# Kernel optimization log

Hardware: AMD Instinct MI355X
Metric: run time of the kernel (lower is better)

Reference implementation:

```python
import jax, jax.numpy as jnp
import numpy as np

S = 7          # grid cells per side (CFG['CELL_NUMS'])
L_COORD = 5.0  # CFG['L_COORD']
L_NOOBJ = 0.5  # CFG['L_NOOBJ']
N_BATCH = 16384


def setup_inputs() -> dict:
    key = jax.random.key(0)
    k1, k2, k3 = jax.random.split(key, 3)
    pred = jax.random.uniform(k1, (N_BATCH, S, S, 30), dtype=jnp.float32)
    target = jax.random.uniform(k2, (N_BATCH, S, S, 30), dtype=jnp.float32)
    obj = jax.random.uniform(k3, (N_BATCH, S, S)) < 0.3
    target = target.at[..., 4].set(jnp.where(obj, target[..., 4], 0.0))
    target = target.at[..., 9].set(jnp.where(obj, target[..., 9], 0.0))
    return {"pred_tensor": pred, "target_tensor": target}


def _yolo_v1_loss(pred, target):
    # pred/target: [N, S, S, 30] = [2 boxes x (x,y,w,h,c), 20 class probs]
    N = pred.shape[0]
    coo_f = (target[..., 4] > 0).astype(pred.dtype)   # [N,S,S] object cells
    noo_f = 1.0 - coo_f                                # no-object cells

    # no-object loss: confidence channels 4 and 9 on noo cells (sum-MSE)
    nooobj_loss = jnp.sum(
        noo_f * ((pred[..., 4] - target[..., 4]) ** 2
                 + (pred[..., 9] - target[..., 9]) ** 2))

    # class loss over object cells (sum-MSE over 20 classes)
    class_loss = jnp.sum(coo_f[..., None] * (pred[..., 10:] - target[..., 10:]) ** 2)

    # boxes: [N,S,S,2,5]
    pb = pred[..., :10].reshape(N, S, S, 2, 5)
    tb = target[..., :10].reshape(N, S, S, 2, 5)

    # xywh -> xyxy for the 2 predicted boxes and the first target box per cell
    p_lt = pb[..., :2] - 0.5 * pb[..., 2:4]
    p_rb = pb[..., :2] + 0.5 * pb[..., 2:4]
    t0 = tb[..., 0, :]                                 # target box used for IOU
    t_lt = t0[..., :2] - 0.5 * t0[..., 2:4]
    t_rb = t0[..., :2] + 0.5 * t0[..., 2:4]

    # NOTE: faithful reproduction of the source's compute_iou, including its
    # bug: wh = (rb - lt < 0).float(), so 'inter' is an indicator product.
    lt = jnp.maximum(p_lt, t_lt[..., None, :])         # [N,S,S,2,2]
    rb = jnp.minimum(p_rb, t_rb[..., None, :])
    wh_ind = (rb - lt < 0).astype(pred.dtype)
    inter = wh_ind[..., 0] * wh_ind[..., 1]            # [N,S,S,2]
    area1 = (p_rb[..., 0] - p_lt[..., 0]) * (p_rb[..., 1] - p_lt[..., 1])
    area2 = ((t_rb[..., 0] - t_lt[..., 0]) * (t_rb[..., 1] - t_lt[..., 1]))[..., None]
    iou = inter / (area1 + area2 - inter)              # [N,S,S,2]

    # responsible box = argmax IOU over the 2 predicted boxes per cell
    idx = jnp.argmax(iou, axis=-1)                     # [N,S,S]
    gather = idx[..., None, None]                      # [N,S,S,1,1]
    resp_p = jnp.take_along_axis(pb, gather, axis=3)[..., 0, :]  # [N,S,S,5]
    resp_t = jnp.take_along_axis(tb, gather, axis=3)[..., 0, :]

    contain_loss = jnp.sum(coo_f * (resp_p[..., 4] - resp_t[..., 4]) ** 2)

    # guard sqrt at masked-out cells so 0*d(sqrt(0)) does not produce NaN grads
    safe = coo_f[..., None] > 0
    sqrt_wp = jnp.sqrt(jnp.where(safe, resp_p[..., 2:4], 1.0))
    sqrt_wt = jnp.sqrt(jnp.where(safe, resp_t[..., 2:4], 1.0))
    loc_loss = (jnp.sum(coo_f[..., None] * (resp_p[..., :2] - resp_t[..., :2]) ** 2)
                + jnp.sum(coo_f[..., None] * (sqrt_wp - sqrt_wt) ** 2))

    return (L_COORD * loc_loss + contain_loss + L_NOOBJ * nooobj_loss + class_loss) / N


def reference(pred_tensor, target_tensor):
    return _yolo_v1_loss(pred_tensor, target_tensor)
```

## Files before the change

### kernel.cpp

```cpp
#include <hip/hip_runtime.h>


#define CH 30
#define CELLS_PER_BLOCK 256
#define BLOCK_THREADS 256
#define FLOATS_PER_BLOCK (CELLS_PER_BLOCK * CH)
#define VEC4_PER_BLOCK (FLOATS_PER_BLOCK / 4)
#define N_BATCH_F 16384.0f

__global__ __launch_bounds__(BLOCK_THREADS)
void yolo_partial(const float* __restrict__ pred,
                  const float* __restrict__ targ,
                  float* __restrict__ partial,
                  int n_cells) {
    __shared__ float sp[FLOATS_PER_BLOCK];
    __shared__ float st[FLOATS_PER_BLOCK];
    __shared__ float wave_sums[BLOCK_THREADS / 64];

    const int tid = threadIdx.x;
    const int cell0 = blockIdx.x * CELLS_PER_BLOCK;
    const int ncell_here = min(CELLS_PER_BLOCK, n_cells - cell0);
    const long long fbase = (long long)cell0 * CH;

    if (ncell_here == CELLS_PER_BLOCK) {
        const float4* gp = (const float4*)(pred + fbase);
        const float4* gt = (const float4*)(targ + fbase);
        float4* lp = (float4*)sp;
        float4* lt4 = (float4*)st;
        for (int v = tid; v < VEC4_PER_BLOCK; v += BLOCK_THREADS) {
            lp[v] = gp[v];
            lt4[v] = gt[v];
        }
    } else {
        const int nflt = ncell_here * CH;
        for (int v = tid; v < nflt; v += BLOCK_THREADS) {
            sp[v] = pred[fbase + v];
            st[v] = targ[fbase + v];
        }
    }
    __syncthreads();

    float sum = 0.0f;
    if (tid < ncell_here) {
        const float* p = &sp[tid * CH];
        const float* t = &st[tid * CH];

        const float t4 = t[4];
        const float t9 = t[9];
        const float coo = (t4 > 0.0f) ? 1.0f : 0.0f;
        const float noo = 1.0f - coo;

        {
            const float d4 = p[4] - t4;
            const float d9 = p[9] - t9;
            sum += 0.5f * noo * (d4 * d4 + d9 * d9);
        }

        if (coo > 0.0f) {
            float cl = 0.0f;
#pragma unroll
            for (int c = 10; c < 30; ++c) {
                const float d = p[c] - t[c];
                cl += d * d;
            }
            sum += cl;

            const float t0x = t[0], t0y = t[1], t0w = t[2], t0h = t[3];
            const float tltx = t0x - 0.5f * t0w;
            const float tlty = t0y - 0.5f * t0h;
            const float trbx = t0x + 0.5f * t0w;
            const float trby = t0y + 0.5f * t0h;
            const float area2 = (trbx - tltx) * (trby - tlty);

            float iou0, iou1;
#pragma unroll
            for (int b = 0; b < 2; ++b) {
                const float* pb = p + b * 5;
                const float pltx = pb[0] - 0.5f * pb[2];
                const float plty = pb[1] - 0.5f * pb[3];
                const float prbx = pb[0] + 0.5f * pb[2];
                const float prby = pb[1] + 0.5f * pb[3];
                const float ltx = fmaxf(pltx, tltx);
                const float lty = fmaxf(plty, tlty);
                const float rbx = fminf(prbx, trbx);
                const float rby = fminf(prby, trby);
                const float wind = (rbx - ltx < 0.0f) ? 1.0f : 0.0f;
                const float hind = (rby - lty < 0.0f) ? 1.0f : 0.0f;
                const float inter = wind * hind;
                const float area1 = (prbx - pltx) * (prby - plty);
                const float iou = inter / (area1 + area2 - inter);
                if (b == 0) iou0 = iou; else iou1 = iou;
            }
            const int idx = (iou1 > iou0) ? 1 : 0;
            const float* rp = p + idx * 5;
            const float* rt = t + idx * 5;

            const float dc = rp[4] - rt[4];
            sum += dc * dc;

            const float dx = rp[0] - rt[0];
            const float dy = rp[1] - rt[1];
            const float dw = sqrtf(rp[2]) - sqrtf(rt[2]);
            const float dh = sqrtf(rp[3]) - sqrtf(rt[3]);
            sum += 5.0f * (dx * dx + dy * dy + dw * dw + dh * dh);
        }
    }

#pragma unroll
    for (int off = 32; off > 0; off >>= 1)
        sum += __shfl_down(sum, off, 64);
    const int wave = tid >> 6;
    const int lane = tid & 63;
    if (lane == 0) wave_sums[wave] = sum;
    __syncthreads();
    if (tid == 0) {
        float tot = 0.0f;
#pragma unroll
        for (int w = 0; w < BLOCK_THREADS / 64; ++w) tot += wave_sums[w];
        partial[blockIdx.x] = tot;
    }
}

__global__ __launch_bounds__(256)
void yolo_reduce(const float* __restrict__ partial, int n, float* __restrict__ out) {
    __shared__ float wave_sums[4];
    float s = 0.0f;
    for (int i = threadIdx.x; i < n; i += 256)
        s += partial[i];
#pragma unroll
    for (int off = 32; off > 0; off >>= 1)
        s += __shfl_down(s, off, 64);
    const int wave = threadIdx.x >> 6;
    const int lane = threadIdx.x & 63;
    if (lane == 0) wave_sums[wave] = s;
    __syncthreads();
    if (threadIdx.x == 0) {
        float tot = wave_sums[0] + wave_sums[1] + wave_sums[2] + wave_sums[3];
        out[0] = tot * (1.0f / N_BATCH_F);
    }
}

extern "C" void kernel_launch(void* const* d_in, const int* in_sizes, int n_in,
                              void* d_out, int out_size, void* d_ws, size_t ws_size,
                              hipStream_t stream) {
    const float* pred = (const float*)d_in[0];
    const float* targ = (const float*)d_in[1];
    float* out = (float*)d_out;
    float* partial = (float*)d_ws;

    const int n_cells = in_sizes[0] / CH;
    const int blocks = (n_cells + CELLS_PER_BLOCK - 1) / CELLS_PER_BLOCK;

    yolo_partial<<<blocks, BLOCK_THREADS, 0, stream>>>(pred, targ, partial, n_cells);
    yolo_reduce<<<1, 256, 0, stream>>>(partial, blocks, out);
}
```

Measured before the change: 209.6 us.

## Use direct global-to-LDS loads with a single reused tile and register-held targets

Result: faster. 204.2 us (-2.6%).

```diff
diff --git a/kernel.cpp b/kernel.cpp
--- a/kernel.cpp
+++ b/kernel.cpp
@@ -2,106 +2,130 @@
 
 
 #define CH 30
-#define CELLS_PER_BLOCK 256
-#define BLOCK_THREADS 256
-#define FLOATS_PER_BLOCK (CELLS_PER_BLOCK * CH)
-#define VEC4_PER_BLOCK (FLOATS_PER_BLOCK / 4)
-#define N_BATCH_F 16384.0f
+#define CPB 256
+#define T 256
+#define TILE_F (CPB * CH)
+#define TILE_V4 (TILE_F / 4)
 
-__global__ __launch_bounds__(BLOCK_THREADS)
+typedef __attribute__((address_space(3))) void* lds_vp;
+typedef const __attribute__((address_space(1))) void* gvp;
+
+__global__ __launch_bounds__(T, 4)
 void yolo_partial(const float* __restrict__ pred,
                   const float* __restrict__ targ,
-                  float* __restrict__ partial,
-                  int n_cells) {
-    __shared__ float sp[FLOATS_PER_BLOCK];
-    __shared__ float st[FLOATS_PER_BLOCK];
-    __shared__ float wave_sums[BLOCK_THREADS / 64];
+                  float* __restrict__ partial) {
+    __shared__ float tile[TILE_F];
+    __shared__ float wave_sums[T / 64];
 
     const int tid = threadIdx.x;
-    const int cell0 = blockIdx.x * CELLS_PER_BLOCK;
-    const int ncell_here = min(CELLS_PER_BLOCK, n_cells - cell0);
-    const long long fbase = (long long)cell0 * CH;
+    const long long fbase = (long long)blockIdx.x * TILE_F;
 
-    if (ncell_here == CELLS_PER_BLOCK) {
+    {
+        const float4* gt = (const float4*)(targ + fbase);
+#pragma unroll
+        for (int k = 0; k < 8; ++k) {
+            const int v = tid + k * T;
+            if (v < TILE_V4)
+                __builtin_amdgcn_global_load_lds((gvp)(gt + v), (lds_vp)(tile + v * 4),
+                                                 16, 0, 0);
+        }
+    }
+    __syncthreads();
+
+    float2 t01, t23, t45, t67, t89, tc[10];
+    {
+        const float2* t2 = (const float2*)(tile + tid * CH);
+        t01 = t2[0]; t23 = t2[1]; t45 = t2[2]; t67 = t2[3]; t89 = t2[4];
+#pragma unroll
+        for (int k = 0; k < 10; ++k) tc[k] = t2[5 + k];
+    }
+    __syncthreads();
+
+    {
         const float4* gp = (const float4*)(pred + fbase);
-        const float4* gt = (const float4*)(targ + fbase);
-        float4* lp = (float4*)sp;
-        float4* lt4 = (float4*)st;
-        for (int v = tid; v < VEC4_PER_BLOCK; v += BLOCK_THREADS) {
-            lp[v] = gp[v];
-            lt4[v] = gt[v];
-        }
-    } else {
-        const int nflt = ncell_here * CH;
-        for (int v = tid; v < nflt; v += BLOCK_THREADS) {
-            sp[v] = pred[fbase + v];
-            st[v] = targ[fbase + v];
+#pragma unroll
+        for (int k = 0; k < 8; ++k) {
+            const int v = tid + k * T;
+            if (v < TILE_V4)
+                __builtin_amdgcn_global_load_lds((gvp)(gp + v), (lds_vp)(tile + v * 4),
+                                                 16, 0, 0);
         }
     }
     __syncthreads();
 
     float sum = 0.0f;
-    if (tid < ncell_here) {
-        const float* p = &sp[tid * CH];
-        const float* t = &st[tid * CH];
+    {
+        const float2* p2 = (const float2*)(tile + tid * CH);
+        const float2 p01 = p2[0], p23 = p2[1], p45 = p2[2], p67 = p2[3], p89 = p2[4];
 
-        const float t4 = t[4];
-        const float t9 = t[9];
-        const float coo = (t4 > 0.0f) ? 1.0f : 0.0f;
-        const float noo = 1.0f - coo;
+        const float t4 = t45.x, t9 = t89.y;
+        const bool coo = t4 > 0.0f;
 
-        {
-            const float d4 = p[4] - t4;
-            const float d9 = p[9] - t9;
-            sum += 0.5f * noo * (d4 * d4 + d9 * d9);
-        }
+        const float d4 = p45.x - t4;
+        const float d9 = p89.y - t9;
+        sum = coo ? 0.0f : 0.5f * (d4 * d4 + d9 * d9);
 
-        if (coo > 0.0f) {
+        if (coo) {
             float cl = 0.0f;
 #pragma unroll
-            for (int c = 10; c < 30; ++c) {
-                const float d = p[c] - t[c];
-                cl += d * d;
+            for (int k = 0; k < 10; ++k) {
+                const float2 pc = p2[5 + k];
+                const float dx = pc.x - tc[k].x;
+                const float dy = pc.y - tc[k].y;
+                cl += dx * dx + dy * dy;
             }
             sum += cl;
 
-            const float t0x = t[0], t0y = t[1], t0w = t[2], t0h = t[3];
-            const float tltx = t0x - 0.5f * t0w;
-            const float tlty = t0y - 0.5f * t0h;
-            const float trbx = t0x + 0.5f * t0w;
-            const float trby = t0y + 0.5f * t0h;
+            const float tltx = t01.x - 0.5f * t23.x;
+            const float tlty = t01.y - 0.5f * t23.y;
+            const float trbx = t01.x + 0.5f * t23.x;
+            const float trby = t01.y + 0.5f * t23.y;
             const float area2 = (trbx - tltx) * (trby - tlty);
 
+            const float b0x = p01.x, b0y = p01.y, b0w = p23.x, b0h = p23.y;
+            const float b1x = p45.y, b1y = p67.x, b1w = p67.y, b1h = p89.x;
+
             float iou0, iou1;
-#pragma unroll
-            for (int b = 0; b < 2; ++b) {
-                const float* pb = p + b * 5;
-                const float pltx = pb[0] - 0.5f * pb[2];
-                const float plty = pb[1] - 0.5f * pb[3];
-                const float prbx = pb[0] + 0.5f * pb[2];
-                const float prby = pb[1] + 0.5f * pb[3];
-                const float ltx = fmaxf(pltx, tltx);
-                const float lty = fmaxf(plty, tlty);
-                const float rbx = fminf(prbx, trbx);
-                const float rby = fminf(prby, trby);
-                const float wind = (rbx - ltx < 0.0f) ? 1.0f : 0.0f;
-                const float hind = (rby - lty < 0.0f) ? 1.0f : 0.0f;
-                const float inter = wind * hind;
+            {
+                const float pltx = b0x - 0.5f * b0w, plty = b0y - 0.5f * b0h;
+                const float prbx = b0x + 0.5f * b0w, prby = b0y + 0.5f * b0h;
+                const float ltx = fmaxf(pltx, tltx), lty = fmaxf(plty, tlty);
+                const float rbx = fminf(prbx, trbx), rby = fminf(prby, trby);
+                const float inter = ((rbx - ltx < 0.0f) ? 1.0f : 0.0f) *
+                                    ((rby - lty < 0.0f) ? 1.0f : 0.0f);
                 const float area1 = (prbx - pltx) * (prby - plty);
-                const float iou = inter / (area1 + area2 - inter);
-                if (b == 0) iou0 = iou; else iou1 = iou;
+                iou0 = inter / (area1 + area2 - inter);
             }
-            const int idx = (iou1 > iou0) ? 1 : 0;
-            const float* rp = p + idx * 5;
-            const float* rt = t + idx * 5;
+            {
+                const float pltx = b1x - 0.5f * b1w, plty = b1y - 0.5f * b1h;
+                const float prbx = b1x + 0.5f * b1w, prby = b1y + 0.5f * b1h;
+                const float ltx = fmaxf(pltx, tltx), lty = fmaxf(plty, tlty);
+                const float rbx = fminf(prbx, trbx), rby = fminf(prby, trby);
+                const float inter = ((rbx - ltx < 0.0f) ? 1.0f : 0.0f) *
+                                    ((rby - lty < 0.0f) ? 1.0f : 0.0f);
+                const float area1 = (prbx - pltx) * (prby - plty);
+                iou1 = inter / (area1 + area2 - inter);
+            }
+            const bool idx1 = iou1 > iou0;
 
-            const float dc = rp[4] - rt[4];
+            const float rpx = idx1 ? b1x : b0x;
+            const float rpy = idx1 ? b1y : b0y;
+            const float rpw = idx1 ? b1w : b0w;
+            const float rph = idx1 ? b1h : b0h;
+            const float rpc = idx1 ? p89.y : p45.x;
+            const float rtx = idx1 ? t45.y : t01.x;
+            const float rty = idx1 ? t67.x : t01.y;
+            const float rtw = idx1 ? t67.y : t23.x;
+            const float rth = idx1 ? t89.x : t23.y;
+            const float rtc = idx1 ? t89.y : t45.x;
+
+            const float dc = rpc - rtc;
             sum += dc * dc;
 
-            const float dx = rp[0] - rt[0];
-            const float dy = rp[1] - rt[1];
-            const float dw = sqrtf(rp[2]) - sqrtf(rt[2]);
-            const float dh = sqrtf(rp[3]) - sqrtf(rt[3]);
+            const float dx = rpx - rtx;
+            const float dy = rpy - rty;
+            const float dw = sqrtf(rpw) - sqrtf(rtw);
+            const float dh = sqrtf(rph) - sqrtf(rth);
             sum += 5.0f * (dx * dx + dy * dy + dw * dw + dh * dh);
         }
     }
@@ -116,7 +140,7 @@
     if (tid == 0) {
         float tot = 0.0f;
 #pragma unroll
-        for (int w = 0; w < BLOCK_THREADS / 64; ++w) tot += wave_sums[w];
+        for (int w = 0; w < T / 64; ++w) tot += wave_sums[w];
         partial[blockIdx.x] = tot;
     }
 }
@@ -125,8 +149,14 @@
 void yolo_reduce(const float* __restrict__ partial, int n, float* __restrict__ out) {
     __shared__ float wave_sums[4];
     float s = 0.0f;
-    for (int i = threadIdx.x; i < n; i += 256)
-        s += partial[i];
+    const int n4 = n >> 2;
+    const float4* p4 = (const float4*)partial;
+    for (int v = threadIdx.x; v < n4; v += 256) {
+        const float4 x = p4[v];
+        s += (x.x + x.y) + (x.z + x.w);
+    }
+    for (int v = (n4 << 2) + threadIdx.x; v < n; v += 256)
+        s += partial[v];
 #pragma unroll
     for (int off = 32; off > 0; off >>= 1)
         s += __shfl_down(s, off, 64);
@@ -135,8 +165,8 @@
     if (lane == 0) wave_sums[wave] = s;
     __syncthreads();
     if (threadIdx.x == 0) {
-        float tot = wave_sums[0] + wave_sums[1] + wave_sums[2] + wave_sums[3];
-        out[0] = tot * (1.0f / N_BATCH_F);
+        const float tot = wave_sums[0] + wave_sums[1] + wave_sums[2] + wave_sums[3];
+        out[0] = tot * (1.0f / 16384.0f);
     }
 }
 
@@ -149,8 +179,8 @@
     float* partial = (float*)d_ws;
 
     const int n_cells = in_sizes[0] / CH;
-    const int blocks = (n_cells + CELLS_PER_BLOCK - 1) / CELLS_PER_BLOCK;
+    const int blocks = n_cells / CPB;
 
-    yolo_partial<<<blocks, BLOCK_THREADS, 0, stream>>>(pred, targ, partial, n_cells);
+    yolo_partial<<<blocks, T, 0, stream>>>(pred, targ, partial);
     yolo_reduce<<<1, 256, 0, stream>>>(partial, blocks, out);
 }
```

## Load cell pairs directly into registers via float4, drop shared-memory staging

Applied to the files above, without the earlier changes.

New measurement: 263.2 us. 1.26x slower.

```diff
diff --git a/kernel.cpp b/kernel.cpp
--- a/kernel.cpp
+++ b/kernel.cpp
@@ -2,109 +2,87 @@
 
 
 #define CH 30
-#define CELLS_PER_BLOCK 256
-#define BLOCK_THREADS 256
-#define FLOATS_PER_BLOCK (CELLS_PER_BLOCK * CH)
-#define VEC4_PER_BLOCK (FLOATS_PER_BLOCK / 4)
-#define N_BATCH_F 16384.0f
 
-__global__ __launch_bounds__(BLOCK_THREADS)
+__device__ __forceinline__ float cell_loss(const float* __restrict__ t,
+                                           const float* __restrict__ p) {
+    const float t4 = t[4];
+    const bool coo = t4 > 0.0f;
+
+    const float d4 = p[4] - t4;
+    const float d9 = p[9] - t[9];
+    float sum = coo ? 0.0f : 0.5f * (d4 * d4 + d9 * d9);
+
+    if (coo) {
+        float cl = 0.0f;
+#pragma unroll
+        for (int c = 10; c < 30; ++c) {
+            const float d = p[c] - t[c];
+            cl += d * d;
+        }
+        sum += cl;
+
+        const float tltx = t[0] - 0.5f * t[2];
+        const float tlty = t[1] - 0.5f * t[3];
+        const float trbx = t[0] + 0.5f * t[2];
+        const float trby = t[1] + 0.5f * t[3];
+        const float area2 = (trbx - tltx) * (trby - tlty);
+
+        float iou0, iou1;
+#pragma unroll
+        for (int b = 0; b < 2; ++b) {
+            const float bx = p[b * 5 + 0], by = p[b * 5 + 1];
+            const float bw = p[b * 5 + 2], bh = p[b * 5 + 3];
+            const float pltx = bx - 0.5f * bw, plty = by - 0.5f * bh;
+            const float prbx = bx + 0.5f * bw, prby = by + 0.5f * bh;
+            const float ltx = fmaxf(pltx, tltx), lty = fmaxf(plty, tlty);
+            const float rbx = fminf(prbx, trbx), rby = fminf(prby, trby);
+            const float inter = ((rbx - ltx < 0.0f) ? 1.0f : 0.0f) *
+                                ((rby - lty < 0.0f) ? 1.0f : 0.0f);
+            const float area1 = (prbx - pltx) * (prby - plty);
+            const float iou = inter / (area1 + area2 - inter);
+            if (b == 0) iou0 = iou; else iou1 = iou;
+        }
+        const int o = (iou1 > iou0) ? 5 : 0;
+
+        const float dc = p[o + 4] - t[o + 4];
+        sum += dc * dc;
+
+        const float dx = p[o + 0] - t[o + 0];
+        const float dy = p[o + 1] - t[o + 1];
+        const float dw = sqrtf(p[o + 2]) - sqrtf(t[o + 2]);
+        const float dh = sqrtf(p[o + 3]) - sqrtf(t[o + 3]);
+        sum += 5.0f * (dx * dx + dy * dy + dw * dw + dh * dh);
+    }
+    return sum;
+}
+
+__global__ __launch_bounds__(256, 3)
 void yolo_partial(const float* __restrict__ pred,
                   const float* __restrict__ targ,
-                  float* __restrict__ partial,
-                  int n_cells) {
-    __shared__ float sp[FLOATS_PER_BLOCK];
-    __shared__ float st[FLOATS_PER_BLOCK];
-    __shared__ float wave_sums[BLOCK_THREADS / 64];
+                  float* __restrict__ partial) {
+    __shared__ float wave_sums[4];
 
     const int tid = threadIdx.x;
-    const int cell0 = blockIdx.x * CELLS_PER_BLOCK;
-    const int ncell_here = min(CELLS_PER_BLOCK, n_cells - cell0);
-    const long long fbase = (long long)cell0 * CH;
+    const long long pair = (long long)blockIdx.x * 256 + tid;
 
-    if (ncell_here == CELLS_PER_BLOCK) {
-        const float4* gp = (const float4*)(pred + fbase);
-        const float4* gt = (const float4*)(targ + fbase);
-        float4* lp = (float4*)sp;
-        float4* lt4 = (float4*)st;
-        for (int v = tid; v < VEC4_PER_BLOCK; v += BLOCK_THREADS) {
-            lp[v] = gp[v];
-            lt4[v] = gt[v];
-        }
-    } else {
-        const int nflt = ncell_here * CH;
-        for (int v = tid; v < nflt; v += BLOCK_THREADS) {
-            sp[v] = pred[fbase + v];
-            st[v] = targ[fbase + v];
-        }
+    const float4* t4 = (const float4*)targ + pair * 15;
+    const float4* p4 = (const float4*)pred + pair * 15;
+
+    float tv[60], pv[60];
+#pragma unroll
+    for (int i = 0; i < 15; ++i) {
+        const float4 v = t4[i];
+        tv[4 * i + 0] = v.x; tv[4 * i + 1] = v.y;
+        tv[4 * i + 2] = v.z; tv[4 * i + 3] = v.w;
     }
-    __syncthreads();
+#pragma unroll
+    for (int i = 0; i < 15; ++i) {
+        const float4 v = p4[i];
+        pv[4 * i + 0] = v.x; pv[4 * i + 1] = v.y;
+        pv[4 * i + 2] = v.z; pv[4 * i + 3] = v.w;
+    }
 
-    float sum = 0.0f;
-    if (tid < ncell_here) {
-        const float* p = &sp[tid * CH];
-        const float* t = &st[tid * CH];
-
-        const float t4 = t[4];
-        const float t9 = t[9];
-        const float coo = (t4 > 0.0f) ? 1.0f : 0.0f;
-        const float noo = 1.0f - coo;
-
-        {
-            const float d4 = p[4] - t4;
-            const float d9 = p[9] - t9;
-            sum += 0.5f * noo * (d4 * d4 + d9 * d9);
-        }
-
-        if (coo > 0.0f) {
-            float cl = 0.0f;
-#pragma unroll
-            for (int c = 10; c < 30; ++c) {
-                const float d = p[c] - t[c];
-                cl += d * d;
-            }
-            sum += cl;
-
-            const float t0x = t[0], t0y = t[1], t0w = t[2], t0h = t[3];
-            const float tltx = t0x - 0.5f * t0w;
-            const float tlty = t0y - 0.5f * t0h;
-            const float trbx = t0x + 0.5f * t0w;
-            const float trby = t0y + 0.5f * t0h;
-            const float area2 = (trbx - tltx) * (trby - tlty);
-
-            float iou0, iou1;
-#pragma unroll
-            for (int b = 0; b < 2; ++b) {
-                const float* pb = p + b * 5;
-                const float pltx = pb[0] - 0.5f * pb[2];
-                const float plty = pb[1] - 0.5f * pb[3];
-                const float prbx = pb[0] + 0.5f * pb[2];
-                const float prby = pb[1] + 0.5f * pb[3];
-                const float ltx = fmaxf(pltx, tltx);
-                const float lty = fmaxf(plty, tlty);
-                const float rbx = fminf(prbx, trbx);
-                const float rby = fminf(prby, trby);
-                const float wind = (rbx - ltx < 0.0f) ? 1.0f : 0.0f;
-                const float hind = (rby - lty < 0.0f) ? 1.0f : 0.0f;
-                const float inter = wind * hind;
-                const float area1 = (prbx - pltx) * (prby - plty);
-                const float iou = inter / (area1 + area2 - inter);
-                if (b == 0) iou0 = iou; else iou1 = iou;
-            }
-            const int idx = (iou1 > iou0) ? 1 : 0;
-            const float* rp = p + idx * 5;
-            const float* rt = t + idx * 5;
-
-            const float dc = rp[4] - rt[4];
-            sum += dc * dc;
-
-            const float dx = rp[0] - rt[0];
-            const float dy = rp[1] - rt[1];
-            const float dw = sqrtf(rp[2]) - sqrtf(rt[2]);
-            const float dh = sqrtf(rp[3]) - sqrtf(rt[3]);
-            sum += 5.0f * (dx * dx + dy * dy + dw * dw + dh * dh);
-        }
-    }
+    float sum = cell_loss(tv, pv) + cell_loss(tv + CH, pv + CH);
 
 #pragma unroll
     for (int off = 32; off > 0; off >>= 1)
@@ -114,10 +92,8 @@
     if (lane == 0) wave_sums[wave] = sum;
     __syncthreads();
     if (tid == 0) {
-        float tot = 0.0f;
-#pragma unroll
-        for (int w = 0; w < BLOCK_THREADS / 64; ++w) tot += wave_sums[w];
-        partial[blockIdx.x] = tot;
+        partial[blockIdx.x] = (wave_sums[0] + wave_sums[1]) +
+                              (wave_sums[2] + wave_sums[3]);
     }
 }
 
@@ -125,8 +101,14 @@
 void yolo_reduce(const float* __restrict__ partial, int n, float* __restrict__ out) {
     __shared__ float wave_sums[4];
     float s = 0.0f;
-    for (int i = threadIdx.x; i < n; i += 256)
-        s += partial[i];
+    const int n4 = n >> 2;
+    const float4* p4 = (const float4*)partial;
+    for (int v = threadIdx.x; v < n4; v += 256) {
+        const float4 x = p4[v];
+        s += (x.x + x.y) + (x.z + x.w);
+    }
+    for (int v = (n4 << 2) + threadIdx.x; v < n; v += 256)
+        s += partial[v];
 #pragma unroll
     for (int off = 32; off > 0; off >>= 1)
         s += __shfl_down(s, off, 64);
@@ -135,8 +117,8 @@
     if (lane == 0) wave_sums[wave] = s;
     __syncthreads();
     if (threadIdx.x == 0) {
-        float tot = wave_sums[0] + wave_sums[1] + wave_sums[2] + wave_sums[3];
-        out[0] = tot * (1.0f / N_BATCH_F);
+        const float tot = wave_sums[0] + wave_sums[1] + wave_sums[2] + wave_sums[3];
+        out[0] = tot * (1.0f / 16384.0f);
     }
 }
 
@@ -149,8 +131,9 @@
     float* partial = (float*)d_ws;
 
     const int n_cells = in_sizes[0] / CH;
-    const int blocks = (n_cells + CELLS_PER_BLOCK - 1) / CELLS_PER_BLOCK;
+    const int n_pairs = n_cells / 2;
+    const int blocks = n_pairs / 256;
 
-    yolo_partial<<<blocks, BLOCK_THREADS, 0, stream>>>(pred, targ, partial, n_cells);
+    yolo_partial<<<blocks, 256, 0, stream>>>(pred, targ, partial);
     yolo_reduce<<<1, 256, 0, stream>>>(partial, blocks, out);
 }
```
